# Performance work log

Measured on AMD Instinct MI355X. Metric: run time of the kernel, lower is better.

## Reference

```python
import jax, jax.numpy as jnp
import numpy as np

H = 2880
E = 8
K = 2
FF = 2880
CLIP = 7.0
AUX_COEF = 0.01
INIT_STD = 0.02
B, T = 2, 1024


def setup_inputs() -> dict:
    key = jax.random.key(0)
    ks = jax.random.split(key, 4)
    x = jax.random.normal(ks[0], (B, T, H), dtype=jnp.float32)
    W_in = INIT_STD * jax.random.normal(ks[1], (E, H, 2 * FF), dtype=jnp.float32)
    b_in = jnp.zeros((E, 2 * FF), dtype=jnp.float32)
    W_out = INIT_STD * jax.random.normal(ks[2], (E, FF, H), dtype=jnp.float32)
    b_out = jnp.zeros((E, H), dtype=jnp.float32)
    router_w = INIT_STD * jax.random.normal(ks[3], (E, H), dtype=jnp.float32)
    router_b = jnp.zeros((E,), dtype=jnp.float32)
    return {"x": x, "W_in": W_in, "b_in": b_in, "W_out": W_out,
            "b_out": b_out, "router_w": router_w, "router_b": router_b}


def reference(x, W_in, b_in, W_out, b_out, router_w, router_b):
    Bx, Tx, Hx = x.shape
    x_flat = x.reshape(-1, Hx)                       # [S, H]
    logits = x_flat @ router_w.T + router_b          # [S, E]

    topk_w, topk_idx = jax.lax.top_k(logits, K)      # [S, K]
    topk_w = jax.nn.softmax(topk_w.astype(jnp.float32), axis=-1).astype(x.dtype)
    one_hot = jax.nn.one_hot(topk_idx, E, dtype=x.dtype)        # [S, K, E]
    final_w = (one_hot * topk_w[..., None]).sum(axis=1)          # [S, E]

    probs = jax.nn.softmax(logits.astype(jnp.float32), axis=-1)  # [S, E]
    importance = probs.mean(axis=0)
    load = final_w.astype(jnp.float32).mean(axis=0)
    aux_loss = AUX_COEF * E * (importance * load).sum()

    # Dense over all experts (as in the original module)
    expert_in = jnp.einsum('sh,ehd->sed', x_flat, W_in) + b_in   # [S, E, 2FF]
    up, gate = jnp.split(expert_in, 2, axis=-1)
    up = jnp.clip(up, -CLIP, CLIP)
    gate = jnp.clip(gate, -CLIP, CLIP)
    act = jax.nn.silu(gate) * up                                 # [S, E, FF]
    expert_out = jnp.einsum('sef,efh->seh', act, W_out) + b_out  # [S, E, H]
    out = jnp.einsum('seh,se->sh', expert_out, final_w).reshape(Bx, Tx, Hx)

    expert_utilization = final_w.mean(axis=0)
    router_entropy = -(probs * jnp.log(probs + 1e-10)).sum(axis=-1).mean()
    return out, aux_loss, expert_utilization, router_entropy
```

## Files before the change

kernel.cpp:

```cpp
#include <hip/hip_runtime.h>
#include <hip/hip_bf16.h>
#include <cstdint>
#include <cstddef>

#define H_ 2880
#define E_ 8
#define FF_ 2880
#define TWO_FF 5760
#define S_ 2048
#define NPAD 5120
#define CLIPV 7.0f
#define AUXC 0.01f
#define NKB 45

#define GRIDP  22112
#define GRID1C 5120
#define GRID2  640

typedef __attribute__((ext_vector_type(8))) short bf16x8;
typedef __attribute__((ext_vector_type(4))) float f32x4;

#define WS_COUNTS   0
#define WS_BASEP    64
#define WS_NS       104
#define WS_SCHED_E  128
#define WS_SCHED_C  5248
#define WS_SCHED_R  10368
#define WS_SCH2_E   15488
#define WS_SCH2_C   18048
#define WS_SCH2_R   20608
#define WS_IDX2     23168
#define WS_W2       39552
#define WS_PROBS    55936
#define WS_ENT      121472
#define WS_TOKL     129664
#define WS_ASSW     150144
#define WS_AG       262144
#define WS_TIN      29753344
#define WS_ACT      295174144
#define WS_TOUT     324665344

typedef const __attribute__((address_space(1))) void global_cvoid;
typedef __attribute__((address_space(3))) void lds_void;

__device__ __forceinline__ void gload_lds16(const void* g, void* l) {
  __builtin_amdgcn_global_load_lds((global_cvoid*)g, (lds_void*)l, 16, 0, 0);
}

__device__ __forceinline__ unsigned int pack2bf(float a, float b) {
  __hip_bfloat162 h = __float22bfloat162_rn(make_float2(a, b));
  union { __hip_bfloat162 h; unsigned int u; } c; c.h = h; return c.u;
}

__device__ __forceinline__ unsigned short f2bf1(float f) {
  __hip_bfloat16 h = __float2bfloat16(f);
  union { __hip_bfloat16 h; unsigned short u; } c; c.h = h; return c.u;
}

__device__ __forceinline__ int xcd_lid(int bid, int ns) {
  int q = ns >> 3, r = ns & 7;
  int xcd = bid & 7, i = bid >> 3;
  int cnt = q + (xcd < r ? 1 : 0);
  if (i >= cnt) return -1;
  return xcd * q + (xcd < r ? xcd : r) + i;
}

template <int LD>
__device__ __forceinline__ void convw_body(const float* __restrict__ src,
                                           unsigned short* __restrict__ dst,
                                           float (*ls)[97]) {
  int tid = threadIdx.x;
#pragma unroll
  for (int i = 0; i < 6; ++i) {
    int u = tid + 256 * i;
    int r = u / 24, c4 = u % 24;
    float4 v = *(const float4*)(src + (size_t)r * LD + c4 * 4);
    ls[r][c4 * 4 + 0] = v.x; ls[r][c4 * 4 + 1] = v.y;
    ls[r][c4 * 4 + 2] = v.z; ls[r][c4 * 4 + 3] = v.w;
  }
  __syncthreads();
#pragma unroll
  for (int i = 0; i < 3; ++i) {
    int ci = tid + 256 * i;
    int kq = ci / 96, n = ci % 96;
    float f[8];
#pragma unroll
    for (int j = 0; j < 8; ++j) f[j] = ls[kq * 8 + j][n];
    uint4 o;
    o.x = pack2bf(f[0], f[1]); o.y = pack2bf(f[2], f[3]);
    o.z = pack2bf(f[4], f[5]); o.w = pack2bf(f[6], f[7]);
    *(uint4*)(dst + ci * 8) = o;
  }
}

__global__ __launch_bounds__(256) void k_pre(
    const float* __restrict__ Win, unsigned short* __restrict__ Tin,
    const float* __restrict__ x, const float* __restrict__ rw,
    const float* __restrict__ rb, int* __restrict__ counts,
    int* __restrict__ idx2, float* __restrict__ wtop,
    float* __restrict__ probs, float* __restrict__ ent) {
  __shared__ float ls[64][97];
  int bid = blockIdx.x;
  if (bid >= 512) {
    int cid = bid - 512;
    int e = cid / 2700, r = cid % 2700, nt = r / 45, kb = r % 45;
    const float* src = Win + (size_t)e * H_ * TWO_FF + (size_t)kb * 64 * TWO_FF + nt * 96;
    unsigned short* dst = Tin + (((size_t)e * 60 + nt) * 45 + kb) * 6144;
    convw_body<TWO_FF>(src, dst, ls);
    return;
  }
  int wave = threadIdx.x >> 6, lane = threadIdx.x & 63;
  int s = bid * 4 + wave;
  if (s >= S_) return;
  const float* xr = x + (size_t)s * H_;
  float acc[E_];
#pragma unroll
  for (int e = 0; e < E_; ++e) acc[e] = 0.f;
  for (int k = lane; k < H_; k += 64) {
    float xv = xr[k];
#pragma unroll
    for (int e = 0; e < E_; ++e) acc[e] = fmaf(xv, rw[e * H_ + k], acc[e]);
  }
#pragma unroll
  for (int e = 0; e < E_; ++e) {
#pragma unroll
    for (int off = 32; off > 0; off >>= 1) acc[e] += __shfl_xor(acc[e], off, 64);
    acc[e] += rb[e];
  }
  if (lane == 0) {
    int i1 = 0; float v1 = acc[0];
#pragma unroll
    for (int e = 1; e < E_; ++e) if (acc[e] > v1) { v1 = acc[e]; i1 = e; }
    int i2 = -1; float v2 = -3.4e38f;
#pragma unroll
    for (int e = 0; e < E_; ++e) if (e != i1 && acc[e] > v2) { v2 = acc[e]; i2 = e; }
    float w1 = 1.f / (1.f + expf(v2 - v1));
    float w2v = 1.f - w1;
    float m = v1;
    float se = 0.f; float p[E_];
#pragma unroll
    for (int e = 0; e < E_; ++e) { p[e] = expf(acc[e] - m); se += p[e]; }
    float inv = 1.f / se; float ents = 0.f;
#pragma unroll
    for (int e = 0; e < E_; ++e) {
      p[e] *= inv;
      ents -= p[e] * logf(p[e] + 1e-10f);
      probs[(size_t)s * E_ + e] = p[e];
    }
    ent[s] = ents;
    idx2[2 * s] = i1; idx2[2 * s + 1] = i2;
    wtop[2 * s] = w1; wtop[2 * s + 1] = w2v;
    atomicAdd(&counts[i1], 1); atomicAdd(&counts[i2], 1);
  }
}

__global__ void k_finalize(const int* __restrict__ counts, const float* __restrict__ probs,
                           const float* __restrict__ ent, const int* __restrict__ idx2,
                           const float* __restrict__ wtop, float* __restrict__ outsc,
                           int* __restrict__ basep, int* __restrict__ sched_e,
                           int* __restrict__ sched_c, int* __restrict__ sched_r,
                           int* __restrict__ s2e, int* __restrict__ s2c,
                           int* __restrict__ s2r, int* __restrict__ nsp,
                           int* __restrict__ tokl, float* __restrict__ assw) {
  __shared__ float red[256];
  __shared__ float tot[17];
  __shared__ int sh_tc[8], sh_cum[9], sh_base[9], sfill[8];
  int t = threadIdx.x;
  float imp[8], ld[8]; float es = 0.f;
#pragma unroll
  for (int e = 0; e < 8; ++e) { imp[e] = 0.f; ld[e] = 0.f; }
  for (int s = t; s < S_; s += 256) {
#pragma unroll
    for (int e = 0; e < 8; ++e) imp[e] += probs[(size_t)s * 8 + e];
    es += ent[s];
    int e0 = idx2[2 * s], e1 = idx2[2 * s + 1];
    float a = wtop[2 * s], b = wtop[2 * s + 1];
#pragma unroll
    for (int e = 0; e < 8; ++e)
      ld[e] += (e0 == e ? a : 0.f) + (e1 == e ? b : 0.f);
  }
#pragma unroll
  for (int q = 0; q < 17; ++q) {
    float v = (q < 8) ? imp[q] : ((q < 16) ? ld[q - 8] : es);
    red[t] = v; __syncthreads();
    for (int o = 128; o > 0; o >>= 1) { if (t < o) red[t] += red[t + o]; __syncthreads(); }
    if (t == 0) tot[q] = red[0];
    __syncthreads();
  }
  if (t == 0) {
    float aux = 0.f;
#pragma unroll
    for (int e = 0; e < 8; ++e) aux += (tot[e] / (float)S_) * (tot[8 + e] / (float)S_);
    aux *= AUXC * (float)E_;
    outsc[0] = aux;
#pragma unroll
    for (int e = 0; e < 8; ++e) outsc[1 + e] = tot[8 + e] / (float)S_;
    outsc[9] = tot[16] / (float)S_;
    int bp = 0, cum = 0;
    for (int e = 0; e < 8; ++e) {
      int tc = (counts[e] + 127) >> 7;
      sh_tc[e] = tc; sh_cum[e] = cum; sh_base[e] = bp;
      basep[e] = bp;
      cum += tc; bp += tc << 7;
    }
    sh_cum[8] = cum; sh_base[8] = bp; basep[8] = bp;
    nsp[0] = cum * 30; nsp[1] = cum * 15;
  }
  if (t < 8) sfill[t] = 0;
  __syncthreads();
  int ntile = sh_cum[8];
  int ns1 = ntile * 30;
  for (int sidx = t; sidx < ns1; sidx += 256) {
    int e = 0;
    while (e < 7 && sidx >= sh_cum[e + 1] * 30) ++e;
    int tc = sh_tc[e];
    int rem = sidx - sh_cum[e] * 30;
    int col = rem / tc, tt = rem - col * tc;
    sched_e[sidx] = e; sched_c[sidx] = col; sched_r[sidx] = tt * 128;
  }
  int ns2 = ntile * 15;
  for (int sidx = t; sidx < ns2; sidx += 256) {
    int e = 0;
    while (e < 7 && sidx >= sh_cum[e + 1] * 15) ++e;
    int tc = sh_tc[e];
    int rem = sidx - sh_cum[e] * 15;
    int col = rem / tc, tt = rem - col * tc;
    s2e[sidx] = e; s2c[sidx] = col; s2r[sidx] = tt * 128;
  }
  for (int s = t; s < S_; s += 256) {
#pragma unroll
    for (int k = 0; k < 2; ++k) {
      int e = idx2[2 * s + k];
      int p = sh_base[e] + atomicAdd(&sfill[e], 1);
      tokl[p] = s;
      assw[p] = wtop[2 * s + k];
    }
  }
}

__global__ void k_gather(const float* __restrict__ x, const int* __restrict__ tokl,
                         unsigned short* __restrict__ Ag) {
  int g = blockIdx.x;
  int tok = tokl[g];
  int tm = g >> 7, r = g & 127;
  unsigned short* dst = Ag + (size_t)tm * 45 * 8192;
  const float* src = x + (size_t)tok * H_;
  for (int c = threadIdx.x; c < 360; c += 256) {
    float4 v0 = *(const float4*)(src + c * 8);
    float4 v1 = *(const float4*)(src + c * 8 + 4);
    uint4 o;
    o.x = pack2bf(v0.x, v0.y); o.y = pack2bf(v0.z, v0.w);
    o.z = pack2bf(v1.x, v1.y); o.w = pack2bf(v1.z, v1.w);
    *(uint4*)(dst + (size_t)(c >> 3) * 8192 + (c & 7) * 1024 + r * 8) = o;
  }
}

__global__ __launch_bounds__(256, 2) void k_gemm1c(
    const unsigned short* __restrict__ Ag, const unsigned short* __restrict__ Tin,
    const float* __restrict__ bin, const int* __restrict__ sched_e,
    const int* __restrict__ sched_c, const int* __restrict__ sched_r,
    const int* __restrict__ basep, const int* __restrict__ counts,
    const int* __restrict__ nsp, unsigned short* __restrict__ act,
    const float* __restrict__ Wout, unsigned short* __restrict__ Tout) {
  __shared__ __align__(16) char lds[81920];
  int bid = blockIdx.x;
  int g = bid >> 5, p = bid & 31, phase = g & 3;
  if ((p & 3) != phase) {
    int nless = (p >> 2) + (((p & 3) > phase) ? 1 : 0);
    int cid = g * 24 + (p - nless);
    float (*ls)[97] = (float(*)[97])lds;
    for (int tile = cid; tile < 10800; tile += 3840) {
      int e = tile / 1350, r2 = tile % 1350, nt = r2 / 45, kb = r2 % 45;
      const float* src = Wout + (size_t)e * FF_ * H_ + (size_t)kb * 64 * H_ + nt * 96;
      unsigned short* dst = Tout + (((size_t)e * 30 + nt) * 45 + kb) * 6144;
      convw_body<H_>(src, dst, ls);
      __syncthreads();
    }
    return;
  }
  int lid = g * 8 + (p >> 2);
  if (lid >= nsp[0]) return;
  int e = sched_e[lid], col = sched_c[lid], row0 = sched_r[lid];
  int n_e = counts[e], rbase = basep[e];
  int n0 = col * 96;
  int tid = threadIdx.x, lane = tid & 63, wv = tid >> 6;
  int wm = wv >> 1, wn = wv & 1;
  int tile_m = (rbase + row0) >> 7;

  const char* abase  = (const char*)Ag  + (size_t)tile_m * 45 * 16384;
  const char* bubase = (const char*)Tin + (((size_t)e * 60 + col) * 45) * 12288;
  const char* bgbase = (const char*)Tin + (((size_t)e * 60 + col + 30) * 45) * 12288;

#define ST1(BUF, KT) do {                                                        \
  const char* at_ = abase + (size_t)(KT) * 16384;                                \
  const char* bu_ = bubase + (size_t)(KT) * 12288;                               \
  const char* bg_ = bgbase + (size_t)(KT) * 12288;                               \
  _Pragma("unroll") for (int i_ = 0; i_ < 4; ++i_)                               \
    gload_lds16(at_ + (wv * 4 + i_) * 1024 + lane * 16,                          \
                lds + (BUF) * 16384 + (wv * 4 + i_) * 1024);                     \
  _Pragma("unroll") for (int i_ = 0; i_ < 3; ++i_) {                             \
    gload_lds16(bu_ + (wv * 3 + i_) * 1024 + lane * 16,                          \
                lds + 32768 + (BUF) * 12288 + (wv * 3 + i_) * 1024);             \
    gload_lds16(bg_ + (wv * 3 + i_) * 1024 + lane * 16,                          \
                lds + 57344 + (BUF) * 12288 + (wv * 3 + i_) * 1024); }           \
} while (0)

  f32x4 aU[4][3], aG[4][3];
#pragma unroll
  for (int m = 0; m < 4; ++m)
#pragma unroll
    for (int n = 0; n < 3; ++n) { aU[m][n] = (f32x4)0.f; aG[m][n] = (f32x4)0.f; }

  ST1(0, 0);
  int cur = 0;
  for (int kt = 0; kt < NKB; ++kt) {
    asm volatile("s_barrier" ::: "memory");
    if (kt + 1 < NKB) {
      ST1(cur ^ 1, kt + 1);
      asm volatile("s_waitcnt vmcnt(10)" ::: "memory");
    } else {
      asm volatile("s_waitcnt vmcnt(0)" ::: "memory");
    }
    asm volatile("s_barrier" ::: "memory");
    const char* Ab  = lds + cur * 16384 + (lane >> 4) * 2048 + (wm * 64 + (lane & 15)) * 16;
    const char* Bub = lds + 32768 + cur * 12288 + (lane >> 4) * 1536 + (wn * 48 + (lane & 15)) * 16;
    const char* Bgb = Bub + 24576;
#pragma unroll
    for (int s = 0; s < 2; ++s) {
      bf16x8 af[4], bu[3], bg[3];
#pragma unroll
      for (int m = 0; m < 4; ++m) af[m] = *(const bf16x8*)(Ab + s * 8192 + m * 256);
#pragma unroll
      for (int n = 0; n < 3; ++n) {
        bu[n] = *(const bf16x8*)(Bub + s * 6144 + n * 256);
        bg[n] = *(const bf16x8*)(Bgb + s * 6144 + n * 256);
      }
#pragma unroll
      for (int n = 0; n < 3; ++n)
#pragma unroll
        for (int m = 0; m < 4; ++m) {
          aU[m][n] = __builtin_amdgcn_mfma_f32_16x16x32_bf16(af[m], bu[n], aU[m][n], 0, 0, 0);
          aG[m][n] = __builtin_amdgcn_mfma_f32_16x16x32_bf16(af[m], bg[n], aG[m][n], 0, 0, 0);
        }
    }
    cur ^= 1;
  }
#undef ST1

  float bias_u[3], bias_g[3];
#pragma unroll
  for (int n = 0; n < 3; ++n) {
    int cidx = n0 + wn * 48 + n * 16 + (lane & 15);
    bias_u[n] = bin[(size_t)e * TWO_FF + cidx];
    bias_g[n] = bin[(size_t)e * TWO_FF + FF_ + cidx];
  }
  unsigned short* atile = act + (size_t)tile_m * 45 * 8192;
#pragma unroll
  for (int m = 0; m < 4; ++m) {
#pragma unroll
    for (int q = 0; q < 4; ++q) {
      int r = wm * 64 + m * 16 + (lane >> 4) * 4 + q;
      if (row0 + r < n_e) {
#pragma unroll
        for (int n = 0; n < 3; ++n) {
          int cidx = n0 + wn * 48 + n * 16 + (lane & 15);
          float u = aU[m][n][q] + bias_u[n];
          float gg = aG[m][n][q] + bias_g[n];
          u = fminf(fmaxf(u, -CLIPV), CLIPV);
          gg = fminf(fmaxf(gg, -CLIPV), CLIPV);
          float sig = 1.f / (1.f + expf(-gg));
          atile[(size_t)(cidx >> 6) * 8192 + ((cidx >> 3) & 7) * 1024 + r * 8 + (cidx & 7)]
              = f2bf1(gg * sig * u);
        }
      }
    }
  }
}

__global__ __launch_bounds__(256, 2) void k_gemm2(
    const unsigned short* __restrict__ act, const unsigned short* __restrict__ Tout,
    const float* __restrict__ bout, const int* __restrict__ s2e,
    const int* __restrict__ s2c, const int* __restrict__ s2r,
    const int* __restrict__ basep, const int* __restrict__ counts,
    const int* __restrict__ nsp, const int* __restrict__ tokl,
    const float* __restrict__ assw, float* __restrict__ out) {
  __shared__ __align__(16) char lds[81920];
  int lid = xcd_lid(blockIdx.x, nsp[1]);
  if (lid < 0) return;
  int e = s2e[lid], col = s2c[lid], row0 = s2r[lid];
  int n_e = counts[e], rbase = basep[e];
  int n0 = col * 192;
  int tid = threadIdx.x, lane = tid & 63, wv = tid >> 6;
  int wm = wv >> 1, wn = wv & 1;
  int tile_m = (rbase + row0) >> 7;

  const char* abase = (const char*)act + (size_t)tile_m * 45 * 16384;
  const char* bbase = (const char*)Tout + (((size_t)e * 30 + col * 2) * 45) * 12288;

#define ST2(BUF, KT) do {                                                        \
  const char* at_ = abase + (size_t)(KT) * 16384;                                \
  _Pragma("unroll") for (int i_ = 0; i_ < 4; ++i_)                               \
    gload_lds16(at_ + (wv * 4 + i_) * 1024 + lane * 16,                          \
                lds + (BUF) * 16384 + (wv * 4 + i_) * 1024);                     \
  _Pragma("unroll") for (int i_ = 0; i_ < 6; ++i_) {                             \
    int ch_ = wv * 6 + i_;                                                       \
    const char* bt_ = bbase + (size_t)(ch_ / 12) * 45 * 12288                    \
                      + (size_t)(KT) * 12288 + (ch_ % 12) * 1024;                \
    gload_lds16(bt_ + lane * 16, lds + 32768 + (BUF) * 24576 + ch_ * 1024); }    \
} while (0)

  f32x4 acc[4][6];
#pragma unroll
  for (int m = 0; m < 4; ++m)
#pragma unroll
    for (int n = 0; n < 6; ++n) acc[m][n] = (f32x4)0.f;

  ST2(0, 0);
  int cur = 0;
  for (int kt = 0; kt < NKB; ++kt) {
    asm volatile("s_barrier" ::: "memory");
    if (kt + 1 < NKB) {
      ST2(cur ^ 1, kt + 1);
      asm volatile("s_waitcnt vmcnt(10)" ::: "memory");
    } else {
      asm volatile("s_waitcnt vmcnt(0)" ::: "memory");
    }
    asm volatile("s_barrier" ::: "memory");
    const char* Ab = lds + cur * 16384 + (lane >> 4) * 2048 + (wm * 64 + (lane & 15)) * 16;
    const char* Bb = lds + 32768 + cur * 24576 + wn * 12288 + (lane >> 4) * 1536 + (lane & 15) * 16;
#pragma unroll
    for (int s = 0; s < 2; ++s) {
      bf16x8 af[4], bf[6];
#pragma unroll
      for (int m = 0; m < 4; ++m) af[m] = *(const bf16x8*)(Ab + s * 8192 + m * 256);
#pragma unroll
      for (int n = 0; n < 6; ++n) bf[n] = *(const bf16x8*)(Bb + s * 6144 + n * 256);
#pragma unroll
      for (int n = 0; n < 6; ++n)
#pragma unroll
        for (int m = 0; m < 4; ++m)
          acc[m][n] = __builtin_amdgcn_mfma_f32_16x16x32_bf16(af[m], bf[n], acc[m][n], 0, 0, 0);
    }
    cur ^= 1;
  }
#undef ST2

  float bb[6];
#pragma unroll
  for (int n = 0; n < 6; ++n)
    bb[n] = bout[(size_t)e * H_ + n0 + wn * 96 + n * 16 + (lane & 15)];
#pragma unroll
  for (int m = 0; m < 4; ++m) {
#pragma unroll
    for (int q = 0; q < 4; ++q) {
      int r = wm * 64 + m * 16 + (lane >> 4) * 4 + q;
      if (row0 + r < n_e) {
        int g = rbase + row0 + r;
        int tok = tokl[g];
        float w = assw[g];
        float* orow = out + (size_t)tok * H_;
#pragma unroll
        for (int n = 0; n < 6; ++n) {
          int cidx = n0 + wn * 96 + n * 16 + (lane & 15);
          atomicAdd(&orow[cidx], w * (acc[m][n][q] + bb[n]));
        }
      }
    }
  }
}

extern "C" void kernel_launch(void* const* d_in, const int* in_sizes, int n_in,
                              void* d_out, int out_size, void* d_ws, size_t ws_size,
                              hipStream_t stream) {
  (void)in_sizes; (void)n_in; (void)ws_size;
  const float* x        = (const float*)d_in[0];
  const float* W_in     = (const float*)d_in[1];
  const float* b_in     = (const float*)d_in[2];
  const float* W_out    = (const float*)d_in[3];
  const float* b_out    = (const float*)d_in[4];
  const float* router_w = (const float*)d_in[5];
  const float* router_b = (const float*)d_in[6];
  float* out = (float*)d_out;
  char* ws = (char*)d_ws;

  int*   counts  = (int*)(ws + WS_COUNTS);
  int*   basep   = (int*)(ws + WS_BASEP);
  int*   nsp     = (int*)(ws + WS_NS);
  int*   sched_e = (int*)(ws + WS_SCHED_E);
  int*   sched_c = (int*)(ws + WS_SCHED_C);
  int*   sched_r = (int*)(ws + WS_SCHED_R);
  int*   s2e     = (int*)(ws + WS_SCH2_E);
  int*   s2c     = (int*)(ws + WS_SCH2_C);
  int*   s2r     = (int*)(ws + WS_SCH2_R);
  int*   idx2    = (int*)(ws + WS_IDX2);
  float* wtop    = (float*)(ws + WS_W2);
  float* probs   = (float*)(ws + WS_PROBS);
  float* ent     = (float*)(ws + WS_ENT);
  int*   tokl    = (int*)(ws + WS_TOKL);
  float* assw    = (float*)(ws + WS_ASSW);
  unsigned short* Ag   = (unsigned short*)(ws + WS_AG);
  unsigned short* Tin  = (unsigned short*)(ws + WS_TIN);
  unsigned short* actp = (unsigned short*)(ws + WS_ACT);
  unsigned short* Tout = (unsigned short*)(ws + WS_TOUT);

  hipMemsetAsync(ws, 0, WS_ASSW, stream);
  hipMemsetAsync(d_out, 0, (size_t)out_size * sizeof(float), stream);

  k_pre<<<GRIDP, 256, 0, stream>>>(W_in, Tin, x, router_w, router_b,
                                   counts, idx2, wtop, probs, ent);
  k_finalize<<<1, 256, 0, stream>>>(counts, probs, ent, idx2, wtop,
                                    out + (size_t)S_ * H_, basep,
                                    sched_e, sched_c, sched_r,
                                    s2e, s2c, s2r, nsp, tokl, assw);
  k_gather<<<NPAD, 256, 0, stream>>>(x, tokl, Ag);
  k_gemm1c<<<GRID1C, 256, 0, stream>>>(Ag, Tin, b_in, sched_e, sched_c, sched_r,
                                       basep, counts, nsp, actp, W_out, Tout);
  k_gemm2<<<GRID2, 256, 0, stream>>>(actp, Tout, b_out, s2e, s2c, s2r,
                                     basep, counts, nsp, tokl, assw, out);
}
```

Measured before the change: 608.6 us.

## Halve K-step and LDS footprint in expert GEMMs to raise occupancy

Both expert GEMM kernels now stage K in 32-wide slices (90 steps instead of 45) so the double-buffered LDS drops from 80KB to 40KB, and launch bounds are raised to allow four blocks per CU. The large workspace memset is shrunk to just the counters, with padding slots of the token list zeroed in finalize instead, and the gather kernel skips padded rows beyond the last expert tile. This aims to improve latency hiding and remove memset and gather overhead, at the cost of twice as many barriers and smaller load batches per iteration, plus register pressure under the tighter launch bound.

```diff
diff --git a/kernel.cpp b/kernel.cpp
--- a/kernel.cpp
+++ b/kernel.cpp
@@ -11,7 +11,7 @@
 #define NPAD 5120
 #define CLIPV 7.0f
 #define AUXC 0.01f
-#define NKB 45
+#define NKS 90
 
 #define GRIDP  22112
 #define GRID1C 5120
@@ -227,6 +227,12 @@
     int col = rem / tc, tt = rem - col * tc;
     s2e[sidx] = e; s2c[sidx] = col; s2r[sidx] = tt * 128;
   }
+#pragma unroll
+  for (int e = 0; e < 8; ++e) {
+    int st = sh_base[e] + counts[e];
+    int en = sh_base[e] + (sh_tc[e] << 7);
+    for (int p = st + t; p < en; p += 256) { tokl[p] = 0; assw[p] = 0.f; }
+  }
   for (int s = t; s < S_; s += 256) {
 #pragma unroll
     for (int k = 0; k < 2; ++k) {
@@ -239,8 +245,9 @@
 }
 
 __global__ void k_gather(const float* __restrict__ x, const int* __restrict__ tokl,
-                         unsigned short* __restrict__ Ag) {
+                         const int* __restrict__ basep, unsigned short* __restrict__ Ag) {
   int g = blockIdx.x;
+  if (g >= basep[8]) return;
   int tok = tokl[g];
   int tm = g >> 7, r = g & 127;
   unsigned short* dst = Ag + (size_t)tm * 45 * 8192;
@@ -255,14 +262,14 @@
   }
 }
 
-__global__ __launch_bounds__(256, 2) void k_gemm1c(
+__global__ __launch_bounds__(256, 4) void k_gemm1c(
     const unsigned short* __restrict__ Ag, const unsigned short* __restrict__ Tin,
     const float* __restrict__ bin, const int* __restrict__ sched_e,
     const int* __restrict__ sched_c, const int* __restrict__ sched_r,
     const int* __restrict__ basep, const int* __restrict__ counts,
     const int* __restrict__ nsp, unsigned short* __restrict__ act,
     const float* __restrict__ Wout, unsigned short* __restrict__ Tout) {
-  __shared__ __align__(16) char lds[81920];
+  __shared__ __align__(16) char lds[40960];
   int bid = blockIdx.x;
   int g = bid >> 5, p = bid & 31, phase = g & 3;
   if ((p & 3) != phase) {
@@ -290,19 +297,34 @@
   const char* abase  = (const char*)Ag  + (size_t)tile_m * 45 * 16384;
   const char* bubase = (const char*)Tin + (((size_t)e * 60 + col) * 45) * 12288;
   const char* bgbase = (const char*)Tin + (((size_t)e * 60 + col + 30) * 45) * 12288;
+  char* ldsA  = lds;
+  char* ldsBu = lds + 16384;
+  char* ldsBg = lds + 28672;
 
 #define ST1(BUF, KT) do {                                                        \
-  const char* at_ = abase + (size_t)(KT) * 16384;                                \
-  const char* bu_ = bubase + (size_t)(KT) * 12288;                               \
-  const char* bg_ = bgbase + (size_t)(KT) * 12288;                               \
-  _Pragma("unroll") for (int i_ = 0; i_ < 4; ++i_)                               \
-    gload_lds16(at_ + (wv * 4 + i_) * 1024 + lane * 16,                          \
-                lds + (BUF) * 16384 + (wv * 4 + i_) * 1024);                     \
-  _Pragma("unroll") for (int i_ = 0; i_ < 3; ++i_) {                             \
-    gload_lds16(bu_ + (wv * 3 + i_) * 1024 + lane * 16,                          \
-                lds + 32768 + (BUF) * 12288 + (wv * 3 + i_) * 1024);             \
-    gload_lds16(bg_ + (wv * 3 + i_) * 1024 + lane * 16,                          \
-                lds + 57344 + (BUF) * 12288 + (wv * 3 + i_) * 1024); }           \
+  int kt64_ = (KT) >> 1, h_ = (KT) & 1;                                          \
+  const char* at_ = abase + (size_t)kt64_ * 16384 + h_ * 8192;                   \
+  const char* bu_ = bubase + (size_t)kt64_ * 12288 + h_ * 6144;                  \
+  const char* bg_ = bgbase + (size_t)kt64_ * 12288 + h_ * 6144;                  \
+  gload_lds16(at_ + (wv * 2 + 0) * 1024 + lane * 16,                             \
+              ldsA + (BUF) * 8192 + (wv * 2 + 0) * 1024);                        \
+  gload_lds16(at_ + (wv * 2 + 1) * 1024 + lane * 16,                             \
+              ldsA + (BUF) * 8192 + (wv * 2 + 1) * 1024);                        \
+  if (wv < 2) {                                                                  \
+    gload_lds16(bu_ + (2 * wv + 0) * 1024 + lane * 16,                           \
+                ldsBu + (BUF) * 6144 + (2 * wv + 0) * 1024);                     \
+    gload_lds16(bu_ + (2 * wv + 1) * 1024 + lane * 16,                           \
+                ldsBu + (BUF) * 6144 + (2 * wv + 1) * 1024);                     \
+    gload_lds16(bg_ + wv * 1024 + lane * 16,                                     \
+                ldsBg + (BUF) * 6144 + wv * 1024);                               \
+  } else {                                                                       \
+    gload_lds16(bu_ + (2 + wv) * 1024 + lane * 16,                               \
+                ldsBu + (BUF) * 6144 + (2 + wv) * 1024);                         \
+    gload_lds16(bg_ + (2 * wv - 2) * 1024 + lane * 16,                           \
+                ldsBg + (BUF) * 6144 + (2 * wv - 2) * 1024);                     \
+    gload_lds16(bg_ + (2 * wv - 1) * 1024 + lane * 16,                           \
+                ldsBg + (BUF) * 6144 + (2 * wv - 1) * 1024);                     \
+  }                                                                              \
 } while (0)
 
   f32x4 aU[4][3], aG[4][3];
@@ -313,36 +335,33 @@
 
   ST1(0, 0);
   int cur = 0;
-  for (int kt = 0; kt < NKB; ++kt) {
+  for (int kt = 0; kt < NKS; ++kt) {
     asm volatile("s_barrier" ::: "memory");
-    if (kt + 1 < NKB) {
+    if (kt + 1 < NKS) {
       ST1(cur ^ 1, kt + 1);
-      asm volatile("s_waitcnt vmcnt(10)" ::: "memory");
+      asm volatile("s_waitcnt vmcnt(5)" ::: "memory");
     } else {
       asm volatile("s_waitcnt vmcnt(0)" ::: "memory");
     }
     asm volatile("s_barrier" ::: "memory");
-    const char* Ab  = lds + cur * 16384 + (lane >> 4) * 2048 + (wm * 64 + (lane & 15)) * 16;
-    const char* Bub = lds + 32768 + cur * 12288 + (lane >> 4) * 1536 + (wn * 48 + (lane & 15)) * 16;
-    const char* Bgb = Bub + 24576;
-#pragma unroll
-    for (int s = 0; s < 2; ++s) {
-      bf16x8 af[4], bu[3], bg[3];
-#pragma unroll
-      for (int m = 0; m < 4; ++m) af[m] = *(const bf16x8*)(Ab + s * 8192 + m * 256);
-#pragma unroll
-      for (int n = 0; n < 3; ++n) {
-        bu[n] = *(const bf16x8*)(Bub + s * 6144 + n * 256);
-        bg[n] = *(const bf16x8*)(Bgb + s * 6144 + n * 256);
+    const char* Ab  = ldsA + cur * 8192 + (lane >> 4) * 2048 + (wm * 64 + (lane & 15)) * 16;
+    const char* Bub = ldsBu + cur * 6144 + (lane >> 4) * 1536 + (wn * 48 + (lane & 15)) * 16;
+    const char* Bgb = ldsBg + cur * 6144 + (lane >> 4) * 1536 + (wn * 48 + (lane & 15)) * 16;
+    bf16x8 af[4], bu[3], bg[3];
+#pragma unroll
+    for (int m = 0; m < 4; ++m) af[m] = *(const bf16x8*)(Ab + m * 256);
+#pragma unroll
+    for (int n = 0; n < 3; ++n) {
+      bu[n] = *(const bf16x8*)(Bub + n * 256);
+      bg[n] = *(const bf16x8*)(Bgb + n * 256);
+    }
+#pragma unroll
+    for (int n = 0; n < 3; ++n)
+#pragma unroll
+      for (int m = 0; m < 4; ++m) {
+        aU[m][n] = __builtin_amdgcn_mfma_f32_16x16x32_bf16(af[m], bu[n], aU[m][n], 0, 0, 0);
+        aG[m][n] = __builtin_amdgcn_mfma_f32_16x16x32_bf16(af[m], bg[n], aG[m][n], 0, 0, 0);
       }
-#pragma unroll
-      for (int n = 0; n < 3; ++n)
-#pragma unroll
-        for (int m = 0; m < 4; ++m) {
-          aU[m][n] = __builtin_amdgcn_mfma_f32_16x16x32_bf16(af[m], bu[n], aU[m][n], 0, 0, 0);
-          aG[m][n] = __builtin_amdgcn_mfma_f32_16x16x32_bf16(af[m], bg[n], aG[m][n], 0, 0, 0);
-        }
-    }
     cur ^= 1;
   }
 #undef ST1
@@ -377,14 +396,14 @@
   }
 }
 
-__global__ __launch_bounds__(256, 2) void k_gemm2(
+__global__ __launch_bounds__(256, 4) void k_gemm2(
     const unsigned short* __restrict__ act, const unsigned short* __restrict__ Tout,
     const float* __restrict__ bout, const int* __restrict__ s2e,
     const int* __restrict__ s2c, const int* __restrict__ s2r,
     const int* __restrict__ basep, const int* __restrict__ counts,
     const int* __restrict__ nsp, const int* __restrict__ tokl,
     const float* __restrict__ assw, float* __restrict__ out) {
-  __shared__ __align__(16) char lds[81920];
+  __shared__ __align__(16) char lds[40960];
   int lid = xcd_lid(blockIdx.x, nsp[1]);
   if (lid < 0) return;
   int e = s2e[lid], col = s2c[lid], row0 = s2r[lid];
@@ -396,17 +415,21 @@
 
   const char* abase = (const char*)act + (size_t)tile_m * 45 * 16384;
   const char* bbase = (const char*)Tout + (((size_t)e * 30 + col * 2) * 45) * 12288;
+  char* ldsA = lds;
+  char* ldsB = lds + 16384;
 
 #define ST2(BUF, KT) do {                                                        \
-  const char* at_ = abase + (size_t)(KT) * 16384;                                \
-  _Pragma("unroll") for (int i_ = 0; i_ < 4; ++i_)                               \
-    gload_lds16(at_ + (wv * 4 + i_) * 1024 + lane * 16,                          \
-                lds + (BUF) * 16384 + (wv * 4 + i_) * 1024);                     \
-  _Pragma("unroll") for (int i_ = 0; i_ < 6; ++i_) {                             \
-    int ch_ = wv * 6 + i_;                                                       \
-    const char* bt_ = bbase + (size_t)(ch_ / 12) * 45 * 12288                    \
-                      + (size_t)(KT) * 12288 + (ch_ % 12) * 1024;                \
-    gload_lds16(bt_ + lane * 16, lds + 32768 + (BUF) * 24576 + ch_ * 1024); }    \
+  int kt64_ = (KT) >> 1, h_ = (KT) & 1;                                          \
+  const char* at_ = abase + (size_t)kt64_ * 16384 + h_ * 8192;                   \
+  gload_lds16(at_ + (wv * 2 + 0) * 1024 + lane * 16,                             \
+              ldsA + (BUF) * 8192 + (wv * 2 + 0) * 1024);                        \
+  gload_lds16(at_ + (wv * 2 + 1) * 1024 + lane * 16,                             \
+              ldsA + (BUF) * 8192 + (wv * 2 + 1) * 1024);                        \
+  _Pragma("unroll") for (int i_ = 0; i_ < 3; ++i_) {                             \
+    int ch_ = wv * 3 + i_;                                                       \
+    const char* bt_ = bbase + (size_t)(ch_ / 6) * 45 * 12288                     \
+                      + (size_t)kt64_ * 12288 + h_ * 6144 + (ch_ % 6) * 1024;    \
+    gload_lds16(bt_ + lane * 16, ldsB + (BUF) * 12288 + ch_ * 1024); }           \
 } while (0)
 
   f32x4 acc[4][6];
@@ -417,30 +440,27 @@
 
   ST2(0, 0);
   int cur = 0;
-  for (int kt = 0; kt < NKB; ++kt) {
+  for (int kt = 0; kt < NKS; ++kt) {
     asm volatile("s_barrier" ::: "memory");
-    if (kt + 1 < NKB) {
+    if (kt + 1 < NKS) {
       ST2(cur ^ 1, kt + 1);
-      asm volatile("s_waitcnt vmcnt(10)" ::: "memory");
+      asm volatile("s_waitcnt vmcnt(5)" ::: "memory");
     } else {
       asm volatile("s_waitcnt vmcnt(0)" ::: "memory");
     }
     asm volatile("s_barrier" ::: "memory");
-    const char* Ab = lds + cur * 16384 + (lane >> 4) * 2048 + (wm * 64 + (lane & 15)) * 16;
-    const char* Bb = lds + 32768 + cur * 24576 + wn * 12288 + (lane >> 4) * 1536 + (lane & 15) * 16;
-#pragma unroll
-    for (int s = 0; s < 2; ++s) {
-      bf16x8 af[4], bf[6];
-#pragma unroll
-      for (int m = 0; m < 4; ++m) af[m] = *(const bf16x8*)(Ab + s * 8192 + m * 256);
-#pragma unroll
-      for (int n = 0; n < 6; ++n) bf[n] = *(const bf16x8*)(Bb + s * 6144 + n * 256);
-#pragma unroll
-      for (int n = 0; n < 6; ++n)
-#pragma unroll
-        for (int m = 0; m < 4; ++m)
-          acc[m][n] = __builtin_amdgcn_mfma_f32_16x16x32_bf16(af[m], bf[n], acc[m][n], 0, 0, 0);
-    }
+    const char* Ab = ldsA + cur * 8192 + (lane >> 4) * 2048 + (wm * 64 + (lane & 15)) * 16;
+    const char* Bb = ldsB + cur * 12288 + wn * 6144 + (lane >> 4) * 1536 + (lane & 15) * 16;
+    bf16x8 af[4], bf[6];
+#pragma unroll
+    for (int m = 0; m < 4; ++m) af[m] = *(const bf16x8*)(Ab + m * 256);
+#pragma unroll
+    for (int n = 0; n < 6; ++n) bf[n] = *(const bf16x8*)(Bb + n * 256);
+#pragma unroll
+    for (int n = 0; n < 6; ++n)
+#pragma unroll
+      for (int m = 0; m < 4; ++m)
+        acc[m][n] = __builtin_amdgcn_mfma_f32_16x16x32_bf16(af[m], bf[n], acc[m][n], 0, 0, 0);
     cur ^= 1;
   }
 #undef ST2
@@ -503,7 +523,7 @@
   unsigned short* actp = (unsigned short*)(ws + WS_ACT);
   unsigned short* Tout = (unsigned short*)(ws + WS_TOUT);
 
-  hipMemsetAsync(ws, 0, WS_ASSW, stream);
+  hipMemsetAsync(ws, 0, 128, stream);
   hipMemsetAsync(d_out, 0, (size_t)out_size * sizeof(float), stream);
 
   k_pre<<<GRIDP, 256, 0, stream>>>(W_in, Tin, x, router_w, router_b,
@@ -512,7 +532,7 @@
                                     out + (size_t)S_ * H_, basep,
                                     sched_e, sched_c, sched_r,
                                     s2e, s2c, s2r, nsp, tokl, assw);
-  k_gather<<<NPAD, 256, 0, stream>>>(x, tokl, Ag);
+  k_gather<<<NPAD, 256, 0, stream>>>(x, tokl, basep, Ag);
   k_gemm1c<<<GRID1C, 256, 0, stream>>>(Ag, Tin, b_in, sched_e, sched_c, sched_r,
                                        basep, counts, nsp, actp, W_out, Tout);
   k_gemm2<<<GRID2, 256, 0, stream>>>(actp, Tout, b_out, s2e, s2c, s2r,
```

Result: slower. 875.2 us (+43.8%).
